# Kernel optimization log

Hardware: AMD Instinct MI355X
Metric: run time of the kernel (lower is better)

## Reference

```python
import jax, jax.numpy as jnp
import numpy as np

B, S, D, E, H, K = 2, 2048, 1024, 8, 4096, 2  # batch, seq, n_embed, num_experts, 4*n_embed, top_k


def setup_inputs() -> dict:
    key = jax.random.key(0)
    ks = jax.random.split(key, 10)
    w = lambda k, shape: (jax.random.normal(k, shape, jnp.float32) * 0.02)
    return {
        "x": jax.random.normal(ks[0], (B, S, D), jnp.float32),
        "noise": jax.random.normal(ks[1], (B, S, E), jnp.float32),  # replaces torch.randn_like
        "Wr": w(ks[2], (D, E)),  # topkroute_linear
        "br": jnp.zeros((E,), jnp.float32),
        "Wn": w(ks[3], (D, E)),  # noise_linear
        "bn": jnp.zeros((E,), jnp.float32),
        "W1": w(ks[4], (E, D, H)),  # per-expert first Linear
        "b1": jnp.zeros((E, H), jnp.float32),
        "W2": w(ks[5], (E, H, D)),  # per-expert second Linear
        "b2": jnp.zeros((E, D), jnp.float32),
    }


def reference(x, noise, Wr, br, Wn, bn, W1, b1, W2, b2):
    # --- NoisyTopkRouter ---
    logits = jnp.einsum('bsd,de->bse', x, Wr) + br
    noise_logits = jnp.einsum('bsd,de->bse', x, Wn) + bn
    noisy_logits = logits + noise * jax.nn.softplus(noise_logits)
    _, topi = jax.lax.top_k(noisy_logits, K)                      # [B,S,K]
    sel = (topi[..., :, None] == jnp.arange(E)).any(axis=-2)      # [B,S,E] bool
    gates = jax.nn.softmax(jnp.where(sel, noisy_logits, -jnp.inf), axis=-1)  # sparse softmax
    softmax_gating = jax.nn.softmax(logits, axis=-1)

    # --- expert dispatch: gate is exactly 0 for non-selected experts, so the
    # masked gather/scatter loop equals a gate-weighted sum over all experts ---
    h = jax.nn.relu(jnp.einsum('bsd,edh->ebsh', x, W1) + b1[:, None, None, :])  # [E,B,S,H]
    y = jnp.einsum('ebsh,ehd->ebsd', h, W2) + b2[:, None, None, :]              # [E,B,S,D]
    final = jnp.einsum('bse,ebsd->bsd', gates, y)
    return final, softmax_gating
```

## Files before the change

kernel.cpp:

```cpp
#include <hip/hip_runtime.h>
#include <stdint.h>

#define T_TOK 4096
#define Dm    1024
#define Em    8
#define Hm    4096
#define NSLOT (2 * T_TOK)
#define KSPLIT 2

typedef __bf16 bf16x8 __attribute__((ext_vector_type(8)));
typedef float  f32x4  __attribute__((ext_vector_type(4)));

__device__ __forceinline__ unsigned short f2bf(float f) {
  union { float f; unsigned int u; } c; c.f = f;
  unsigned int u = c.u;
  unsigned int r = u + 0x7fffu + ((u >> 16) & 1u);
  return (unsigned short)(r >> 16);
}

__device__ __forceinline__ void async16(const void* g, void* l) {
  __builtin_amdgcn_global_load_lds(
      (const __attribute__((address_space(1))) void*)g,
      (__attribute__((address_space(3))) void*)l, 16, 0, 0);
}

__global__ void transpose_cvt_kernel(const float* __restrict__ src,
                                     unsigned short* __restrict__ dst,
                                     int R, int C) {
  __shared__ float tile[32][33];
  const int e = blockIdx.z;
  const float* s = src + (size_t)e * R * C;
  unsigned short* d = dst + (size_t)e * R * C;
  const int c0 = blockIdx.x * 32, r0 = blockIdx.y * 32;
  for (int i = threadIdx.y; i < 32; i += 8)
    tile[i][threadIdx.x] = s[(size_t)(r0 + i) * C + c0 + threadIdx.x];
  __syncthreads();
  for (int i = threadIdx.y; i < 32; i += 8)
    d[(size_t)(c0 + i) * R + r0 + threadIdx.x] = f2bf(tile[threadIdx.x][i]);
}

__global__ void cvt_x_kernel(const float* __restrict__ x, unsigned short* __restrict__ xbf) {
  const int i = blockIdx.x * 256 + threadIdx.x;
  float4 v = ((const float4*)x)[i];
  ushort4 o;
  o.x = f2bf(v.x); o.y = f2bf(v.y); o.z = f2bf(v.z); o.w = f2bf(v.w);
  ((ushort4*)xbf)[i] = o;
}

__global__ __launch_bounds__(256) void router_kernel(
    const float* __restrict__ x, const float* __restrict__ noise,
    const float* __restrict__ Wr, const float* __restrict__ br,
    const float* __restrict__ Wn, const float* __restrict__ bn,
    float* __restrict__ out_gating, int* __restrict__ lists,
    int* __restrict__ counts, int* __restrict__ expt,
    int* __restrict__ pos, float* __restrict__ gsel) {
  const int wave = threadIdx.x >> 6, lane = threadIdx.x & 63;
  const int t = blockIdx.x * 4 + wave;
  const float* xt = x + (size_t)t * Dm;
  float accR[Em] = {}, accN[Em] = {};
  for (int d = lane; d < Dm; d += 64) {
    const float xv = xt[d];
    const float* wr = Wr + d * Em;
    const float* wn = Wn + d * Em;
#pragma unroll
    for (int e = 0; e < Em; e++) { accR[e] += xv * wr[e]; accN[e] += xv * wn[e]; }
  }
#pragma unroll
  for (int e = 0; e < Em; e++)
    for (int off = 32; off > 0; off >>= 1) {
      accR[e] += __shfl_down(accR[e], off, 64);
      accN[e] += __shfl_down(accN[e], off, 64);
    }
  if (lane == 0) {
    float lg[Em], ny[Em];
#pragma unroll
    for (int e = 0; e < Em; e++) {
      lg[e] = accR[e] + br[e];
      float nl = accN[e] + bn[e];
      float sp = fmaxf(nl, 0.f) + log1pf(expf(-fabsf(nl)));
      ny[e] = lg[e] + noise[(size_t)t * Em + e] * sp;
    }
    int i0 = 0;
#pragma unroll
    for (int e = 1; e < Em; e++) if (ny[e] > ny[i0]) i0 = e;
    int i1 = (i0 == 0) ? 1 : 0;
#pragma unroll
    for (int e = 0; e < Em; e++) if (e != i0 && ny[e] > ny[i1]) i1 = e;
    const float e1 = expf(ny[i1] - ny[i0]);
    const float g0 = 1.f / (1.f + e1), g1 = e1 / (1.f + e1);
    float m = lg[0];
#pragma unroll
    for (int e = 1; e < Em; e++) m = fmaxf(m, lg[e]);
    float s = 0.f;
#pragma unroll
    for (int e = 0; e < Em; e++) s += expf(lg[e] - m);
#pragma unroll
    for (int e = 0; e < Em; e++) out_gating[(size_t)t * Em + e] = expf(lg[e] - m) / s;
    int p0 = atomicAdd(&counts[i0], 1); lists[i0 * T_TOK + p0] = t;
    int p1 = atomicAdd(&counts[i1], 1); lists[i1 * T_TOK + p1] = t;
    expt[2 * t] = i0; expt[2 * t + 1] = i1;
    pos[2 * t] = p0;  pos[2 * t + 1] = p1;
    gsel[2 * t] = g0; gsel[2 * t + 1] = g1;
  }
}

__global__ __launch_bounds__(256) void gemm1_kernel(
    const unsigned short* __restrict__ xbf, const unsigned short* __restrict__ w1bf,
    const float* __restrict__ b1, const int* __restrict__ counts,
    const int* __restrict__ lists, unsigned short* __restrict__ hbuf) {
  const int e = blockIdx.z;
  const int cnt = counts[e];
  const int m0 = blockIdx.x * 128;
  if (m0 >= cnt) return;
  const int n0 = blockIdx.y * 128;
  int base = 0;
  for (int i = 0; i < e; i++) base += counts[i];

  __shared__ __align__(16) unsigned short As[2][128 * 32];
  __shared__ __align__(16) unsigned short Bs[2][128 * 32];
  __shared__ int tok[128];

  const int tid = threadIdx.x;
  if (tid < 128) {
    int m = m0 + tid;
    tok[tid] = (m < cnt) ? lists[e * T_TOK + m] : 0;
  }
  __syncthreads();

  const int part = tid & 3;
  const int r0 = tid >> 2;
  const int r1 = r0 + 64;
  const size_t gA0 = (size_t)tok[r0] * Dm + part * 8;
  const size_t gA1 = (size_t)tok[r1] * Dm + part * 8;
  const size_t gB0 = ((size_t)e * Hm + n0 + r0) * Dm + part * 8;
  const size_t gB1 = ((size_t)e * Hm + n0 + r1) * Dm + part * 8;

  const int lane = tid & 63, wv = tid >> 6;
  const int quad = lane >> 4, l15 = lane & 15;
  const int wm = (wv >> 1) * 64, wn = (wv & 1) * 64;
  const int lds_off = wv * 512;

  f32x4 acc[4][4] = {};

  async16(xbf + gA0, As[0] + lds_off);
  async16(xbf + gA1, As[0] + 2048 + lds_off);
  async16(w1bf + gB0, Bs[0] + lds_off);
  async16(w1bf + gB1, Bs[0] + 2048 + lds_off);

  const int NI = Dm / 32;
  for (int it = 0; it < NI; it++) {
    const int cur = it & 1;
    __syncthreads();
    if (it + 1 < NI) {
      const int k0 = (it + 1) * 32;
      const int nb = cur ^ 1;
      async16(xbf + gA0 + k0, As[nb] + lds_off);
      async16(xbf + gA1 + k0, As[nb] + 2048 + lds_off);
      async16(w1bf + gB0 + k0, Bs[nb] + lds_off);
      async16(w1bf + gB1 + k0, Bs[nb] + 2048 + lds_off);
    }
    bf16x8 af[4], bfv[4];
#pragma unroll
    for (int i = 0; i < 4; i++)
      af[i] = *(const bf16x8*)(As[cur] + (wm + i * 16 + l15) * 32 + quad * 8);
#pragma unroll
    for (int j = 0; j < 4; j++)
      bfv[j] = *(const bf16x8*)(Bs[cur] + (wn + j * 16 + l15) * 32 + quad * 8);
#pragma unroll
    for (int i = 0; i < 4; i++)
#pragma unroll
      for (int j = 0; j < 4; j++)
        acc[i][j] = __builtin_amdgcn_mfma_f32_16x16x32_bf16(af[i], bfv[j], acc[i][j], 0, 0, 0);
  }

#pragma unroll
  for (int i = 0; i < 4; i++)
#pragma unroll
    for (int r = 0; r < 4; r++) {
      const int ml = wm + i * 16 + quad * 4 + r;
      const int m = m0 + ml;
      if (m < cnt) {
#pragma unroll
        for (int j = 0; j < 4; j++) {
          const int n = n0 + wn + j * 16 + l15;
          float v = acc[i][j][r] + b1[(size_t)e * Hm + n];
          v = fmaxf(v, 0.f);
          hbuf[(size_t)(base + m) * Hm + n] = f2bf(v);
        }
      }
    }
}

__global__ __launch_bounds__(256) void gemm2_kernel(
    const unsigned short* __restrict__ hbuf, const unsigned short* __restrict__ w2bf,
    const int* __restrict__ counts, float* __restrict__ ybuf) {
  const int e = blockIdx.z >> 1;
  const int ks = blockIdx.z & 1;
  const int cnt = counts[e];
  const int m0 = blockIdx.x * 128;
  if (m0 >= cnt) return;
  const int n0 = blockIdx.y * 128;
  int base = 0;
  for (int i = 0; i < e; i++) base += counts[i];
  const int kbase = ks * (Hm / KSPLIT);

  __shared__ __align__(16) unsigned short As[2][128 * 32];
  __shared__ __align__(16) unsigned short Bs[2][128 * 32];

  const int tid = threadIdx.x;
  const int part = tid & 3;
  const int r0 = tid >> 2;
  const int r1 = r0 + 64;
  const int rowA0 = min(base + m0 + r0, NSLOT - 1);
  const int rowA1 = min(base + m0 + r1, NSLOT - 1);
  const size_t gA0 = (size_t)rowA0 * Hm + kbase + part * 8;
  const size_t gA1 = (size_t)rowA1 * Hm + kbase + part * 8;
  const size_t gB0 = ((size_t)e * Dm + n0 + r0) * Hm + kbase + part * 8;
  const size_t gB1 = ((size_t)e * Dm + n0 + r1) * Hm + kbase + part * 8;

  const int lane = tid & 63, wv = tid >> 6;
  const int quad = lane >> 4, l15 = lane & 15;
  const int wm = (wv >> 1) * 64, wn = (wv & 1) * 64;
  const int lds_off = wv * 512;

  f32x4 acc[4][4] = {};

  async16(hbuf + gA0, As[0] + lds_off);
  async16(hbuf + gA1, As[0] + 2048 + lds_off);
  async16(w2bf + gB0, Bs[0] + lds_off);
  async16(w2bf + gB1, Bs[0] + 2048 + lds_off);

  const int NI = Hm / KSPLIT / 32;
  for (int it = 0; it < NI; it++) {
    const int cur = it & 1;
    __syncthreads();
    if (it + 1 < NI) {
      const int k0 = (it + 1) * 32;
      const int nb = cur ^ 1;
      async16(hbuf + gA0 + k0, As[nb] + lds_off);
      async16(hbuf + gA1 + k0, As[nb] + 2048 + lds_off);
      async16(w2bf + gB0 + k0, Bs[nb] + lds_off);
      async16(w2bf + gB1 + k0, Bs[nb] + 2048 + lds_off);
    }
    bf16x8 af[4], bfv[4];
#pragma unroll
    for (int i = 0; i < 4; i++)
      af[i] = *(const bf16x8*)(As[cur] + (wm + i * 16 + l15) * 32 + quad * 8);
#pragma unroll
    for (int j = 0; j < 4; j++)
      bfv[j] = *(const bf16x8*)(Bs[cur] + (wn + j * 16 + l15) * 32 + quad * 8);
#pragma unroll
    for (int i = 0; i < 4; i++)
#pragma unroll
      for (int j = 0; j < 4; j++)
        acc[i][j] = __builtin_amdgcn_mfma_f32_16x16x32_bf16(af[i], bfv[j], acc[i][j], 0, 0, 0);
  }

  float* yb = ybuf + (size_t)ks * NSLOT * Dm;
#pragma unroll
  for (int i = 0; i < 4; i++)
#pragma unroll
    for (int r = 0; r < 4; r++) {
      const int ml = wm + i * 16 + quad * 4 + r;
      const int m = m0 + ml;
      if (m < cnt) {
#pragma unroll
        for (int j = 0; j < 4; j++) {
          const int n = n0 + wn + j * 16 + l15;
          yb[(size_t)(base + m) * Dm + n] = acc[i][j][r];
        }
      }
    }
}

__global__ __launch_bounds__(256) void combine_kernel(
    const float* __restrict__ ybuf, const float* __restrict__ b2,
    const int* __restrict__ counts, const int* __restrict__ expt,
    const int* __restrict__ pos, const float* __restrict__ gsel,
    float* __restrict__ out) {
  const int t = blockIdx.x;
  const int e0 = expt[2 * t], e1 = expt[2 * t + 1];
  const float g0 = gsel[2 * t], g1 = gsel[2 * t + 1];
  int b0 = 0, b1 = 0;
  for (int i = 0; i < e0; i++) b0 += counts[i];
  for (int i = 0; i < e1; i++) b1 += counts[i];
  const size_t s0 = (size_t)(b0 + pos[2 * t]) * Dm;
  const size_t s1 = (size_t)(b1 + pos[2 * t + 1]) * Dm;
  const size_t half = (size_t)NSLOT * Dm;
  const int c = threadIdx.x * 4;
  float4 y0a = *(const float4*)(ybuf + s0 + c);
  float4 y0b = *(const float4*)(ybuf + half + s0 + c);
  float4 y1a = *(const float4*)(ybuf + s1 + c);
  float4 y1b = *(const float4*)(ybuf + half + s1 + c);
  float4 z0 = *(const float4*)(b2 + (size_t)e0 * Dm + c);
  float4 z1 = *(const float4*)(b2 + (size_t)e1 * Dm + c);
  float4 o;
  o.x = g0 * (y0a.x + y0b.x + z0.x) + g1 * (y1a.x + y1b.x + z1.x);
  o.y = g0 * (y0a.y + y0b.y + z0.y) + g1 * (y1a.y + y1b.y + z1.y);
  o.z = g0 * (y0a.z + y0b.z + z0.z) + g1 * (y1a.z + y1b.z + z1.z);
  o.w = g0 * (y0a.w + y0b.w + z0.w) + g1 * (y1a.w + y1b.w + z1.w);
  *(float4*)(out + (size_t)t * Dm + c) = o;
}

extern "C" void kernel_launch(void* const* d_in, const int* in_sizes, int n_in,
                              void* d_out, int out_size, void* d_ws, size_t ws_size,
                              hipStream_t stream) {
  const float* x     = (const float*)d_in[0];
  const float* noise = (const float*)d_in[1];
  const float* Wr    = (const float*)d_in[2];
  const float* br    = (const float*)d_in[3];
  const float* Wn    = (const float*)d_in[4];
  const float* bn    = (const float*)d_in[5];
  const float* W1    = (const float*)d_in[6];
  const float* b1    = (const float*)d_in[7];
  const float* W2    = (const float*)d_in[8];
  const float* b2    = (const float*)d_in[9];

  float* out        = (float*)d_out;
  float* out_gating = out + (size_t)T_TOK * Dm;

  char* ws = (char*)d_ws;
  unsigned short* w1bf = (unsigned short*)(ws);
  unsigned short* w2bf = (unsigned short*)(ws + 67108864);
  unsigned short* xbf  = (unsigned short*)(ws + 134217728);
  unsigned short* hbuf = (unsigned short*)(ws + 142606336);
  float* ybuf          = (float*)(ws);
  int*   lists         = (int*)(ws + 209715200);
  int*   expt          = (int*)(ws + 209846272);
  int*   pos           = (int*)(ws + 209879040);
  float* gsel          = (float*)(ws + 209911808);
  int*   counts        = (int*)(ws + 209944576);

  hipMemsetAsync(counts, 0, Em * sizeof(int), stream);

  transpose_cvt_kernel<<<dim3(Hm / 32, Dm / 32, Em), dim3(32, 8), 0, stream>>>(W1, w1bf, Dm, Hm);
  transpose_cvt_kernel<<<dim3(Dm / 32, Hm / 32, Em), dim3(32, 8), 0, stream>>>(W2, w2bf, Hm, Dm);
  cvt_x_kernel<<<(T_TOK * Dm / 4) / 256, 256, 0, stream>>>(x, xbf);

  router_kernel<<<T_TOK / 4, 256, 0, stream>>>(x, noise, Wr, br, Wn, bn,
                                               out_gating, lists, counts, expt, pos, gsel);

  gemm1_kernel<<<dim3(16, Hm / 128, Em), 256, 0, stream>>>(xbf, w1bf, b1, counts, lists, hbuf);
  gemm2_kernel<<<dim3(16, Dm / 128, Em * KSPLIT), 256, 0, stream>>>(hbuf, w2bf, counts, ybuf);
  combine_kernel<<<T_TOK, 256, 0, stream>>>(ybuf, b2, counts, expt, pos, gsel, out);
}
```

Baseline: 871.5 us.

## Load GEMM operands directly into registers instead of staging through LDS

```diff
diff --git a/kernel.cpp b/kernel.cpp
--- a/kernel.cpp
+++ b/kernel.cpp
@@ -16,12 +16,6 @@
   unsigned int u = c.u;
   unsigned int r = u + 0x7fffu + ((u >> 16) & 1u);
   return (unsigned short)(r >> 16);
-}
-
-__device__ __forceinline__ void async16(const void* g, void* l) {
-  __builtin_amdgcn_global_load_lds(
-      (const __attribute__((address_space(1))) void*)g,
-      (__attribute__((address_space(3))) void*)l, 16, 0, 0);
 }
 
 __global__ void transpose_cvt_kernel(const float* __restrict__ src,
@@ -104,7 +98,7 @@
   }
 }
 
-__global__ __launch_bounds__(256) void gemm1_kernel(
+__global__ __launch_bounds__(256, 3) void gemm1_kernel(
     const unsigned short* __restrict__ xbf, const unsigned short* __restrict__ w1bf,
     const float* __restrict__ b1, const int* __restrict__ counts,
     const int* __restrict__ lists, unsigned short* __restrict__ hbuf) {
@@ -116,61 +110,53 @@
   int base = 0;
   for (int i = 0; i < e; i++) base += counts[i];
 
-  __shared__ __align__(16) unsigned short As[2][128 * 32];
-  __shared__ __align__(16) unsigned short Bs[2][128 * 32];
-  __shared__ int tok[128];
-
-  const int tid = threadIdx.x;
-  if (tid < 128) {
-    int m = m0 + tid;
-    tok[tid] = (m < cnt) ? lists[e * T_TOK + m] : 0;
-  }
-  __syncthreads();
-
-  const int part = tid & 3;
-  const int r0 = tid >> 2;
-  const int r1 = r0 + 64;
-  const size_t gA0 = (size_t)tok[r0] * Dm + part * 8;
-  const size_t gA1 = (size_t)tok[r1] * Dm + part * 8;
-  const size_t gB0 = ((size_t)e * Hm + n0 + r0) * Dm + part * 8;
-  const size_t gB1 = ((size_t)e * Hm + n0 + r1) * Dm + part * 8;
-
-  const int lane = tid & 63, wv = tid >> 6;
+  const int tid = threadIdx.x, lane = tid & 63, wv = tid >> 6;
   const int quad = lane >> 4, l15 = lane & 15;
   const int wm = (wv >> 1) * 64, wn = (wv & 1) * 64;
-  const int lds_off = wv * 512;
+
+  const unsigned short* aptr[4];
+#pragma unroll
+  for (int i = 0; i < 4; i++) {
+    const int m = m0 + wm + i * 16 + l15;
+    const int t = (m < cnt) ? lists[e * T_TOK + m] : 0;
+    aptr[i] = xbf + (size_t)t * Dm + quad * 8;
+  }
+  const unsigned short* bptr[4];
+#pragma unroll
+  for (int j = 0; j < 4; j++)
+    bptr[j] = w1bf + ((size_t)e * Hm + n0 + wn + j * 16 + l15) * Dm + quad * 8;
 
   f32x4 acc[4][4] = {};
-
-  async16(xbf + gA0, As[0] + lds_off);
-  async16(xbf + gA1, As[0] + 2048 + lds_off);
-  async16(w1bf + gB0, Bs[0] + lds_off);
-  async16(w1bf + gB1, Bs[0] + 2048 + lds_off);
+  bf16x8 a_[2][4], b_[2][4];
+#pragma unroll
+  for (int i = 0; i < 4; i++) {
+    a_[0][i] = *(const bf16x8*)(aptr[i]);
+    b_[0][i] = *(const bf16x8*)(bptr[i]);
+  }
 
   const int NI = Dm / 32;
-  for (int it = 0; it < NI; it++) {
-    const int cur = it & 1;
-    __syncthreads();
-    if (it + 1 < NI) {
-      const int k0 = (it + 1) * 32;
-      const int nb = cur ^ 1;
-      async16(xbf + gA0 + k0, As[nb] + lds_off);
-      async16(xbf + gA1 + k0, As[nb] + 2048 + lds_off);
-      async16(w1bf + gB0 + k0, Bs[nb] + lds_off);
-      async16(w1bf + gB1 + k0, Bs[nb] + 2048 + lds_off);
-    }
-    bf16x8 af[4], bfv[4];
+#pragma unroll 2
+  for (int it = 0; it < NI - 1; it++) {
+    const int cur = it & 1, nxt = cur ^ 1;
+    const int k = (it + 1) * 32;
+#pragma unroll
+    for (int i = 0; i < 4; i++) {
+      a_[nxt][i] = *(const bf16x8*)(aptr[i] + k);
+      b_[nxt][i] = *(const bf16x8*)(bptr[i] + k);
+    }
 #pragma unroll
     for (int i = 0; i < 4; i++)
-      af[i] = *(const bf16x8*)(As[cur] + (wm + i * 16 + l15) * 32 + quad * 8);
-#pragma unroll
-    for (int j = 0; j < 4; j++)
-      bfv[j] = *(const bf16x8*)(Bs[cur] + (wn + j * 16 + l15) * 32 + quad * 8);
+#pragma unroll
+      for (int j = 0; j < 4; j++)
+        acc[i][j] = __builtin_amdgcn_mfma_f32_16x16x32_bf16(a_[cur][i], b_[cur][j], acc[i][j], 0, 0, 0);
+  }
+  {
+    const int lc = (NI - 1) & 1;
 #pragma unroll
     for (int i = 0; i < 4; i++)
 #pragma unroll
       for (int j = 0; j < 4; j++)
-        acc[i][j] = __builtin_amdgcn_mfma_f32_16x16x32_bf16(af[i], bfv[j], acc[i][j], 0, 0, 0);
+        acc[i][j] = __builtin_amdgcn_mfma_f32_16x16x32_bf16(a_[lc][i], b_[lc][j], acc[i][j], 0, 0, 0);
   }
 
 #pragma unroll
@@ -191,7 +177,7 @@
     }
 }
 
-__global__ __launch_bounds__(256) void gemm2_kernel(
+__global__ __launch_bounds__(256, 3) void gemm2_kernel(
     const unsigned short* __restrict__ hbuf, const unsigned short* __restrict__ w2bf,
     const int* __restrict__ counts, float* __restrict__ ybuf) {
   const int e = blockIdx.z >> 1;
@@ -204,56 +190,52 @@
   for (int i = 0; i < e; i++) base += counts[i];
   const int kbase = ks * (Hm / KSPLIT);
 
-  __shared__ __align__(16) unsigned short As[2][128 * 32];
-  __shared__ __align__(16) unsigned short Bs[2][128 * 32];
-
-  const int tid = threadIdx.x;
-  const int part = tid & 3;
-  const int r0 = tid >> 2;
-  const int r1 = r0 + 64;
-  const int rowA0 = min(base + m0 + r0, NSLOT - 1);
-  const int rowA1 = min(base + m0 + r1, NSLOT - 1);
-  const size_t gA0 = (size_t)rowA0 * Hm + kbase + part * 8;
-  const size_t gA1 = (size_t)rowA1 * Hm + kbase + part * 8;
-  const size_t gB0 = ((size_t)e * Dm + n0 + r0) * Hm + kbase + part * 8;
-  const size_t gB1 = ((size_t)e * Dm + n0 + r1) * Hm + kbase + part * 8;
-
-  const int lane = tid & 63, wv = tid >> 6;
+  const int tid = threadIdx.x, lane = tid & 63, wv = tid >> 6;
   const int quad = lane >> 4, l15 = lane & 15;
   const int wm = (wv >> 1) * 64, wn = (wv & 1) * 64;
-  const int lds_off = wv * 512;
+
+  const unsigned short* aptr[4];
+#pragma unroll
+  for (int i = 0; i < 4; i++) {
+    const int mrow = min(base + m0 + wm + i * 16 + l15, NSLOT - 1);
+    aptr[i] = hbuf + (size_t)mrow * Hm + kbase + quad * 8;
+  }
+  const unsigned short* bptr[4];
+#pragma unroll
+  for (int j = 0; j < 4; j++)
+    bptr[j] = w2bf + ((size_t)e * Dm + n0 + wn + j * 16 + l15) * Hm + kbase + quad * 8;
 
   f32x4 acc[4][4] = {};
-
-  async16(hbuf + gA0, As[0] + lds_off);
-  async16(hbuf + gA1, As[0] + 2048 + lds_off);
-  async16(w2bf + gB0, Bs[0] + lds_off);
-  async16(w2bf + gB1, Bs[0] + 2048 + lds_off);
+  bf16x8 a_[2][4], b_[2][4];
+#pragma unroll
+  for (int i = 0; i < 4; i++) {
+    a_[0][i] = *(const bf16x8*)(aptr[i]);
+    b_[0][i] = *(const bf16x8*)(bptr[i]);
+  }
 
   const int NI = Hm / KSPLIT / 32;
-  for (int it = 0; it < NI; it++) {
-    const int cur = it & 1;
-    __syncthreads();
-    if (it + 1 < NI) {
-      const int k0 = (it + 1) * 32;
-      const int nb = cur ^ 1;
-      async16(hbuf + gA0 + k0, As[nb] + lds_off);
-      async16(hbuf + gA1 + k0, As[nb] + 2048 + lds_off);
-      async16(w2bf + gB0 + k0, Bs[nb] + lds_off);
-      async16(w2bf + gB1 + k0, Bs[nb] + 2048 + lds_off);
-    }
-    bf16x8 af[4], bfv[4];
+#pragma unroll 2
+  for (int it = 0; it < NI - 1; it++) {
+    const int cur = it & 1, nxt = cur ^ 1;
+    const int k = (it + 1) * 32;
+#pragma unroll
+    for (int i = 0; i < 4; i++) {
+      a_[nxt][i] = *(const bf16x8*)(aptr[i] + k);
+      b_[nxt][i] = *(const bf16x8*)(bptr[i] + k);
+    }
 #pragma unroll
     for (int i = 0; i < 4; i++)
-      af[i] = *(const bf16x8*)(As[cur] + (wm + i * 16 + l15) * 32 + quad * 8);
-#pragma unroll
-    for (int j = 0; j < 4; j++)
-      bfv[j] = *(const bf16x8*)(Bs[cur] + (wn + j * 16 + l15) * 32 + quad * 8);
+#pragma unroll
+      for (int j = 0; j < 4; j++)
+        acc[i][j] = __builtin_amdgcn_mfma_f32_16x16x32_bf16(a_[cur][i], b_[cur][j], acc[i][j], 0, 0, 0);
+  }
+  {
+    const int lc = (NI - 1) & 1;
 #pragma unroll
     for (int i = 0; i < 4; i++)
 #pragma unroll
       for (int j = 0; j < 4; j++)
-        acc[i][j] = __builtin_amdgcn_mfma_f32_16x16x32_bf16(af[i], bfv[j], acc[i][j], 0, 0, 0);
+        acc[i][j] = __builtin_amdgcn_mfma_f32_16x16x32_bf16(a_[lc][i], b_[lc][j], acc[i][j], 0, 0, 0);
   }
 
   float* yb = ybuf + (size_t)ks * NSLOT * Dm;
```

Result: slower. 1.396 ms (+60.2%).
